# Optimization experiments

Hardware: AMD Instinct MI355X
Metric: run time of the kernel (lower is better)

## Reference

```python
import jax, jax.numpy as jnp
import numpy as np

N = 10000        # total_node
IN_SIZE = 128
OUT_SIZE = 128


def setup_inputs() -> dict:
    key = jax.random.key(0)
    k_adj, k_x, k_wn, k_ws = jax.random.split(key, 4)
    adj = jax.random.uniform(k_adj, (N, N), dtype=jnp.float32)           # package[1]
    old_node_embedding = jax.random.normal(k_x, (N, IN_SIZE), dtype=jnp.float32)
    # nn.Linear weights are stored [out, in]
    W_nei = jax.random.normal(k_wn, (OUT_SIZE, IN_SIZE), dtype=jnp.float32) * (1.0 / np.sqrt(IN_SIZE))
    W_self = jax.random.normal(k_ws, (OUT_SIZE, IN_SIZE), dtype=jnp.float32) * (1.0 / np.sqrt(IN_SIZE))
    return {
        "adj": adj,
        "old_node_embedding": old_node_embedding,
        "W_nei": W_nei,
        "W_self": W_self,
        "out_size": OUT_SIZE,
        "use_divce": 0,
    }


def reference(adj, old_node_embedding, W_nei, W_self, out_size, use_divce):
    # Vectorized form of the per-node torch loop:
    #   nei_gather[n]   = adj[n, :] @ X                (torch.mm per node)
    #   nei_info[n]     = nei_gather[n] @ W_nei^T      (nei_update1)
    #   self_info[n]    = X[n] @ W_self^T              (self_node_update1)
    #   new_emb[n]      = act(nei_info[n] + self_info[n])
    # active_method fixed to tanh.
    nei_gather = adj @ old_node_embedding                         # [N, in]
    nei_info = nei_gather @ W_nei.T                               # [N, out]
    self_info = old_node_embedding @ W_self.T                     # [N, out]
    return jnp.tanh(nei_info + self_info)
```

## Files before the change

kernel.cpp:

```cpp
#include <hip/hip_runtime.h>
#include <cmath>


#define N_NODES 10000
#define EMB 128
#define XNT_STRIDE 10240
#define KC 1280
#define NKCH 8

typedef __bf16 bf16x8 __attribute__((ext_vector_type(8)));
typedef float  f32x4  __attribute__((ext_vector_type(4)));

#define GLOAD_LDS16(gp, lp)                                                  \
    __builtin_amdgcn_global_load_lds(                                        \
        (const __attribute__((address_space(1))) void*)(gp),                 \
        (__attribute__((address_space(3))) void*)(lp), 16, 0, 0)

__device__ __forceinline__ void split8(const float4& x0, const float4& x1,
                                       bf16x8& h, bf16x8& l) {
    float f[8] = {x0.x, x0.y, x0.z, x0.w, x1.x, x1.y, x1.z, x1.w};
#pragma unroll
    for (int i = 0; i < 8; ++i) {
        __bf16 hh = (__bf16)f[i];
        h[i] = hh;
        l[i] = (__bf16)(f[i] - (float)hh);
    }
}

__global__ __launch_bounds__(256) void prep_kernel(
    const float* __restrict__ X, const float* __restrict__ Wn,
    __bf16* __restrict__ xnt_hi, __bf16* __restrict__ xnt_lo)
{
    __shared__ float Xl[32 * EMB];
    const int tid = threadIdx.x;
    const int n0 = blockIdx.x * 32;

    if (blockIdx.x == 0) {
        bf16x8 z;
#pragma unroll
        for (int i = 0; i < 8; ++i) z[i] = (__bf16)0.0f;
        for (int g = tid; g < 128 * 30; g += 256) {
            int col = g / 30, j = g % 30;
            size_t off = (size_t)col * XNT_STRIDE + N_NODES + j * 8;
            *(bf16x8*)(xnt_hi + off) = z;
            *(bf16x8*)(xnt_lo + off) = z;
        }
    }

#pragma unroll
    for (int i = 0; i < 4; ++i) {
        int idx = tid + i * 256;
        int r = idx >> 5;
        int c4 = (idx & 31) << 2;
        int row = n0 + r;
        float4 v = make_float4(0.f, 0.f, 0.f, 0.f);
        if (row < N_NODES) v = *(const float4*)(X + (size_t)row * EMB + c4);
        *(float4*)(Xl + r * EMB + c4) = v;
    }
    __syncthreads();

    const int c = tid & 127;
    const int half = tid >> 7;
    const float* wrow = Wn + c * EMB;

    float acc[16];
#pragma unroll
    for (int r = 0; r < 16; ++r) acc[r] = 0.f;

    for (int k4 = 0; k4 < 32; ++k4) {
        float4 w = *(const float4*)(wrow + k4 * 4);
#pragma unroll
        for (int r = 0; r < 16; ++r) {
            float4 x = *(const float4*)(Xl + (half * 16 + r) * EMB + k4 * 4);
            acc[r] += x.x * w.x + x.y * w.y + x.z * w.z + x.w * w.w;
        }
    }

    if (n0 + half * 16 < N_NODES) {
        bf16x8 h0, h1, l0, l1;
#pragma unroll
        for (int r = 0; r < 16; ++r) {
            float f = acc[r];
            __bf16 h = (__bf16)f;
            __bf16 l = (__bf16)(f - (float)h);
            if (r < 8) { h0[r] = h; l0[r] = l; }
            else       { h1[r - 8] = h; l1[r - 8] = l; }
        }
        size_t base = (size_t)c * XNT_STRIDE + n0 + half * 16;
        *(bf16x8*)(xnt_hi + base)     = h0;
        *(bf16x8*)(xnt_hi + base + 8) = h1;
        *(bf16x8*)(xnt_lo + base)     = l0;
        *(bf16x8*)(xnt_lo + base + 8) = l1;
    }
}

__global__ __launch_bounds__(256, 4) void gemm_kernel(
    const float* __restrict__ adj, const __bf16* __restrict__ xnt_hi,
    const __bf16* __restrict__ xnt_lo, float* __restrict__ Ppart)
{
    __shared__ float  Af [64 * 32];
    __shared__ __bf16 Bhs[128 * 32];
    __shared__ __bf16 Bls[128 * 32];

    const int tid = threadIdx.x;
    const int m0 = blockIdx.x * 64;
    const int kc0 = blockIdx.y * KC;
    const int kc_end = min(kc0 + KC, N_NODES);
    const int nsub = (kc_end - kc0 + 31) >> 5;

    const int lane = tid & 63;
    const int wave = tid >> 6;
    const int wm = (wave & 1) * 32;
    const int wn = (wave >> 1) * 64;
    const int fr = lane & 15;
    const int q  = lane >> 4;
    const int f7 = fr & 7;

    const int a_c4 = ((tid & 7) ^ ((tid >> 3) & 7)) * 4;
    size_t a_rowoff[2];
#pragma unroll
    for (int i = 0; i < 2; ++i) {
        int r = i * 32 + (tid >> 3);
        if (m0 + r >= N_NODES) r &= 15;
        a_rowoff[i] = (size_t)(m0 + r) * N_NODES;
    }
    const int b_k8 = ((tid & 3) ^ ((tid >> 3) & 3)) * 8;
    size_t b_coloff[2];
#pragma unroll
    for (int i = 0; i < 2; ++i)
        b_coloff[i] = (size_t)(i * 64 + (tid >> 2)) * XNT_STRIDE;

    f32x4 acc[2][4];
#pragma unroll
    for (int mt = 0; mt < 2; ++mt)
#pragma unroll
        for (int nt = 0; nt < 4; ++nt)
#pragma unroll
            for (int e = 0; e < 4; ++e) acc[mt][nt][e] = 0.f;

    for (int ks = 0; ks < nsub; ++ks) {
        const int k0 = kc0 + ks * 32;

#pragma unroll
        for (int i = 0; i < 2; ++i) {
            int kk = k0 + a_c4;
            if (kk + 4 > kc_end) kk = kc0;
            GLOAD_LDS16(adj + a_rowoff[i] + kk, Af + (i * 256 + tid) * 4);
        }
#pragma unroll
        for (int i = 0; i < 2; ++i) {
            GLOAD_LDS16(xnt_hi + b_coloff[i] + k0 + b_k8,
                        Bhs + (i * 256 + tid) * 8);
            GLOAD_LDS16(xnt_lo + b_coloff[i] + k0 + b_k8,
                        Bls + (i * 256 + tid) * 8);
        }
        __syncthreads();

        bf16x8 ah[2], al[2], bh[4], bl[4];
#pragma unroll
        for (int mt = 0; mt < 2; ++mt) {
            int r = wm + mt * 16 + fr;
            int c0 = q * 2;
            int pc0 = c0 ^ f7;
            int pc1 = (c0 + 1) ^ f7;
            float4 fa = *(const float4*)(Af + r * 32 + pc0 * 4);
            float4 fb = *(const float4*)(Af + r * 32 + pc1 * 4);
            split8(fa, fb, ah[mt], al[mt]);
        }
#pragma unroll
        for (int nt = 0; nt < 4; ++nt) {
            int col = wn + nt * 16 + fr;
            int pq = q ^ ((fr >> 1) & 3);
            bh[nt] = *(const bf16x8*)(Bhs + col * 32 + pq * 8);
            bl[nt] = *(const bf16x8*)(Bls + col * 32 + pq * 8);
        }
#pragma unroll
        for (int mt = 0; mt < 2; ++mt)
#pragma unroll
            for (int nt = 0; nt < 4; ++nt) {
                acc[mt][nt] = __builtin_amdgcn_mfma_f32_16x16x32_bf16(ah[mt], bh[nt], acc[mt][nt], 0, 0, 0);
                acc[mt][nt] = __builtin_amdgcn_mfma_f32_16x16x32_bf16(ah[mt], bl[nt], acc[mt][nt], 0, 0, 0);
                acc[mt][nt] = __builtin_amdgcn_mfma_f32_16x16x32_bf16(al[mt], bh[nt], acc[mt][nt], 0, 0, 0);
            }

        __syncthreads();
    }

    float* P = Ppart + (size_t)blockIdx.y * ((size_t)N_NODES * EMB);
#pragma unroll
    for (int mt = 0; mt < 2; ++mt) {
        int rbase = m0 + wm + mt * 16 + q * 4;
#pragma unroll
        for (int nt = 0; nt < 4; ++nt) {
            int col = wn + nt * 16 + fr;
#pragma unroll
            for (int r = 0; r < 4; ++r) {
                int row = rbase + r;
                if (row < N_NODES)
                    P[(size_t)row * EMB + col] = acc[mt][nt][r];
            }
        }
    }
}

__global__ __launch_bounds__(256) void epi_kernel(
    const float* __restrict__ X, const float* __restrict__ Wself,
    const float* __restrict__ Ppart, float* __restrict__ out)
{
    __shared__ float Xl[32 * EMB];
    const int tid = threadIdx.x;
    const int n0 = blockIdx.x * 32;

#pragma unroll
    for (int i = 0; i < 4; ++i) {
        int idx = tid + i * 256;
        int r = idx >> 5;
        int c4 = (idx & 31) << 2;
        int row = n0 + r;
        float4 v = make_float4(0.f, 0.f, 0.f, 0.f);
        if (row < N_NODES) v = *(const float4*)(X + (size_t)row * EMB + c4);
        *(float4*)(Xl + r * EMB + c4) = v;
    }
    __syncthreads();

    const int c = tid & 127;
    const int half = tid >> 7;
    const float* wrow = Wself + c * EMB;

    float acc[16];
#pragma unroll
    for (int r = 0; r < 16; ++r) acc[r] = 0.f;

    for (int k4 = 0; k4 < 32; ++k4) {
        float4 w = *(const float4*)(wrow + k4 * 4);
#pragma unroll
        for (int r = 0; r < 16; ++r) {
            float4 x = *(const float4*)(Xl + (half * 16 + r) * EMB + k4 * 4);
            acc[r] += x.x * w.x + x.y * w.y + x.z * w.z + x.w * w.w;
        }
    }

    if (n0 + half * 16 < N_NODES) {
        const size_t rb = (size_t)(n0 + half * 16) * EMB + c;
#pragma unroll
        for (int p = 0; p < NKCH; ++p) {
            const float* Pp = Ppart + (size_t)p * ((size_t)N_NODES * EMB) + rb;
#pragma unroll
            for (int r = 0; r < 16; ++r)
                acc[r] += Pp[(size_t)r * EMB];
        }
#pragma unroll
        for (int r = 0; r < 16; ++r)
            out[rb + (size_t)r * EMB] = tanhf(acc[r]);
    }
}

__global__ __launch_bounds__(256) void gemm0_kernel(
    const float* __restrict__ adj, const float* __restrict__ X,
    float* __restrict__ Y)
{
    __shared__ float As[128 * 33];
    __shared__ float Xs[32 * 132];
    const int tid = threadIdx.x;
    const int m0 = blockIdx.x * 128;
    const int kc0 = blockIdx.y * KC;
    const int kc_end = min(kc0 + KC, N_NODES);
    const int nsub = (kc_end - kc0 + 31) >> 5;

    const int am = tid >> 1, akq = tid & 1;
    const bool arv = (m0 + am) < N_NODES;
    const float* arow_p = adj + (size_t)(m0 + am) * N_NODES;
    const int xr = tid >> 3, xq = tid & 7;
    const int mq = tid >> 4, nq = tid & 15;

    float acc[8][8];
#pragma unroll
    for (int i = 0; i < 8; ++i)
#pragma unroll
        for (int j = 0; j < 8; ++j) acc[i][j] = 0.f;

    for (int ks = 0; ks < nsub; ++ks) {
        int k0 = kc0 + ks * 32;
#pragma unroll
        for (int i = 0; i < 4; ++i) {
            int k = k0 + akq * 16 + i * 4;
            float4 v = make_float4(0.f, 0.f, 0.f, 0.f);
            if (arv && k < kc_end) v = *(const float4*)(arow_p + k);
            float* d = As + am * 33 + akq * 16 + i * 4;
            d[0] = v.x; d[1] = v.y; d[2] = v.z; d[3] = v.w;
        }
#pragma unroll
        for (int i = 0; i < 4; ++i) {
            int c0 = xq * 16 + i * 4;
            int krow = k0 + xr;
            float4 v = make_float4(0.f, 0.f, 0.f, 0.f);
            if (krow < kc_end) v = *(const float4*)(X + (size_t)krow * EMB + c0);
            *(float4*)(Xs + xr * 132 + c0) = v;
        }
        __syncthreads();
        for (int k = 0; k < 32; ++k) {
            float a8[8];
#pragma unroll
            for (int i = 0; i < 8; ++i) a8[i] = As[(mq * 8 + i) * 33 + k];
            float4 x0 = *(const float4*)(Xs + k * 132 + nq * 8);
            float4 x1 = *(const float4*)(Xs + k * 132 + nq * 8 + 4);
            float x8[8] = { x0.x, x0.y, x0.z, x0.w, x1.x, x1.y, x1.z, x1.w };
#pragma unroll
            for (int i = 0; i < 8; ++i)
#pragma unroll
                for (int j = 0; j < 8; ++j) acc[i][j] += a8[i] * x8[j];
        }
        __syncthreads();
    }
#pragma unroll
    for (int i = 0; i < 8; ++i) {
        int row = m0 + mq * 8 + i;
        if (row < N_NODES) {
#pragma unroll
            for (int j = 0; j < 8; ++j)
                atomicAdd(Y + (size_t)row * EMB + nq * 8 + j, acc[i][j]);
        }
    }
}

__global__ __launch_bounds__(256) void epi0_kernel(
    const float* __restrict__ X, const float* __restrict__ Wn,
    const float* __restrict__ Ws, float* __restrict__ out)
{
    __shared__ float Xl[32 * EMB];
    __shared__ float Yl[32 * EMB];
    const int tid = threadIdx.x;
    const int n0 = blockIdx.x * 32;

#pragma unroll
    for (int i = 0; i < 4; ++i) {
        int idx = tid + i * 256;
        int r = idx >> 5;
        int c4 = (idx & 31) << 2;
        int row = n0 + r;
        float4 vx = make_float4(0.f, 0.f, 0.f, 0.f);
        float4 vy = vx;
        if (row < N_NODES) {
            vx = *(const float4*)(X + (size_t)row * EMB + c4);
            vy = *(const float4*)(out + (size_t)row * EMB + c4);
        }
        *(float4*)(Xl + r * EMB + c4) = vx;
        *(float4*)(Yl + r * EMB + c4) = vy;
    }
    __syncthreads();

    const int c = tid & 127;
    const int half = tid >> 7;
    const float* wn = Wn + c * EMB;
    const float* ws = Ws + c * EMB;

    float accn[16], accs[16];
#pragma unroll
    for (int r = 0; r < 16; ++r) { accn[r] = 0.f; accs[r] = 0.f; }

    for (int k4 = 0; k4 < 32; ++k4) {
        float4 a = *(const float4*)(wn + k4 * 4);
        float4 b = *(const float4*)(ws + k4 * 4);
#pragma unroll
        for (int r = 0; r < 16; ++r) {
            float4 y = *(const float4*)(Yl + (half * 16 + r) * EMB + k4 * 4);
            float4 x = *(const float4*)(Xl + (half * 16 + r) * EMB + k4 * 4);
            accn[r] += y.x * a.x + y.y * a.y + y.z * a.z + y.w * a.w;
            accs[r] += x.x * b.x + x.y * b.y + x.z * b.z + x.w * b.w;
        }
    }
#pragma unroll
    for (int r = 0; r < 16; ++r) {
        int row = n0 + half * 16 + r;
        if (row < N_NODES)
            out[(size_t)row * EMB + c] = tanhf(accn[r] + accs[r]);
    }
}

extern "C" void kernel_launch(void* const* d_in, const int* in_sizes, int n_in,
                              void* d_out, int out_size, void* d_ws, size_t ws_size,
                              hipStream_t stream) {
    const float* adj = (const float*)d_in[0];
    const float* X   = (const float*)d_in[1];
    const float* Wn  = (const float*)d_in[2];
    const float* Ws  = (const float*)d_in[3];
    float* out = (float*)d_out;

    const size_t xnt_elems = (size_t)EMB * XNT_STRIDE;
    const size_t xnt_bytes = xnt_elems * 2 * sizeof(unsigned short);
    const size_t part_bytes = (size_t)NKCH * N_NODES * EMB * sizeof(float);

    if (ws_size >= xnt_bytes + part_bytes) {
        __bf16* xh = (__bf16*)d_ws;
        __bf16* xl = xh + xnt_elems;
        float* Ppart = (float*)((char*)d_ws + xnt_bytes);
        prep_kernel<<<(N_NODES + 31) / 32, 256, 0, stream>>>(X, Wn, xh, xl);
        gemm_kernel<<<dim3((N_NODES + 63) / 64, NKCH), 256, 0, stream>>>(adj, xh, xl, Ppart);
        epi_kernel<<<(N_NODES + 31) / 32, 256, 0, stream>>>(X, Ws, Ppart, out);
    } else {
        hipMemsetAsync(d_out, 0, (size_t)N_NODES * EMB * sizeof(float), stream);
        gemm0_kernel<<<dim3((N_NODES + 127) / 128, NKCH), 256, 0, stream>>>(adj, X, out);
        epi0_kernel<<<(N_NODES + 31) / 32, 256, 0, stream>>>(X, Wn, Ws, out);
    }
}
```

Measured before the change: 642.3 us.

## Drop LDS staging in adjacency GEMM, load fragments directly from global memory

The GEMM kernel no longer stages adj and the bf16 hi/lo X tiles in shared memory with global_load_lds and barriers. Each wave now reads its MFMA fragments straight from global memory, and the block tile grows to 128 rows by the full 128 columns, with each wave owning 32 rows across all columns. This removes the LDS round trip and the __syncthreads calls. In exchange, each wave does uncoalesced strided global loads of the B fragments, every wave rereads the same B data and relies on cache, registers per thread rise, and the occupancy hint is dropped.

```diff
diff --git a/kernel.cpp b/kernel.cpp
--- a/kernel.cpp
+++ b/kernel.cpp
@@ -10,11 +10,6 @@
 
 typedef __bf16 bf16x8 __attribute__((ext_vector_type(8)));
 typedef float  f32x4  __attribute__((ext_vector_type(4)));
-
-#define GLOAD_LDS16(gp, lp)                                                  \
-    __builtin_amdgcn_global_load_lds(                                        \
-        (const __attribute__((address_space(1))) void*)(gp),                 \
-        (__attribute__((address_space(3))) void*)(lp), 16, 0, 0)
 
 __device__ __forceinline__ void split8(const float4& x0, const float4& x1,
                                        bf16x8& h, bf16x8& l) {
@@ -94,96 +89,75 @@
     }
 }
 
-__global__ __launch_bounds__(256, 4) void gemm_kernel(
+__global__ __launch_bounds__(256) void gemm_kernel(
     const float* __restrict__ adj, const __bf16* __restrict__ xnt_hi,
     const __bf16* __restrict__ xnt_lo, float* __restrict__ Ppart)
 {
-    __shared__ float  Af [64 * 32];
-    __shared__ __bf16 Bhs[128 * 32];
-    __shared__ __bf16 Bls[128 * 32];
-
-    const int tid = threadIdx.x;
-    const int m0 = blockIdx.x * 64;
+    const int tid = threadIdx.x;
+    const int m0 = blockIdx.x * 128;
     const int kc0 = blockIdx.y * KC;
     const int kc_end = min(kc0 + KC, N_NODES);
     const int nsub = (kc_end - kc0 + 31) >> 5;
 
     const int lane = tid & 63;
     const int wave = tid >> 6;
-    const int wm = (wave & 1) * 32;
-    const int wn = (wave >> 1) * 64;
+    const int wm = wave * 32;
     const int fr = lane & 15;
     const int q  = lane >> 4;
-    const int f7 = fr & 7;
-
-    const int a_c4 = ((tid & 7) ^ ((tid >> 3) & 7)) * 4;
-    size_t a_rowoff[2];
-#pragma unroll
-    for (int i = 0; i < 2; ++i) {
-        int r = i * 32 + (tid >> 3);
-        if (m0 + r >= N_NODES) r &= 15;
-        a_rowoff[i] = (size_t)(m0 + r) * N_NODES;
-    }
-    const int b_k8 = ((tid & 3) ^ ((tid >> 3) & 3)) * 8;
-    size_t b_coloff[2];
-#pragma unroll
-    for (int i = 0; i < 2; ++i)
-        b_coloff[i] = (size_t)(i * 64 + (tid >> 2)) * XNT_STRIDE;
-
-    f32x4 acc[2][4];
+
+    const float* arow[2];
+#pragma unroll
+    for (int mt = 0; mt < 2; ++mt) {
+        int r = m0 + wm + mt * 16 + fr;
+        if (r >= N_NODES) r = 0;
+        arow[mt] = adj + (size_t)r * N_NODES;
+    }
+
+    size_t bcol[8];
+#pragma unroll
+    for (int nt = 0; nt < 8; ++nt)
+        bcol[nt] = (size_t)(nt * 16 + fr) * XNT_STRIDE;
+
+    f32x4 acc[2][8];
 #pragma unroll
     for (int mt = 0; mt < 2; ++mt)
 #pragma unroll
-        for (int nt = 0; nt < 4; ++nt)
+        for (int nt = 0; nt < 8; ++nt)
 #pragma unroll
             for (int e = 0; e < 4; ++e) acc[mt][nt][e] = 0.f;
 
     for (int ks = 0; ks < nsub; ++ks) {
         const int k0 = kc0 + ks * 32;
-
-#pragma unroll
-        for (int i = 0; i < 2; ++i) {
-            int kk = k0 + a_c4;
-            if (kk + 4 > kc_end) kk = kc0;
-            GLOAD_LDS16(adj + a_rowoff[i] + kk, Af + (i * 256 + tid) * 4);
-        }
-#pragma unroll
-        for (int i = 0; i < 2; ++i) {
-            GLOAD_LDS16(xnt_hi + b_coloff[i] + k0 + b_k8,
-                        Bhs + (i * 256 + tid) * 8);
-            GLOAD_LDS16(xnt_lo + b_coloff[i] + k0 + b_k8,
-                        Bls + (i * 256 + tid) * 8);
-        }
-        __syncthreads();
-
-        bf16x8 ah[2], al[2], bh[4], bl[4];
+        const int ka = k0 + q * 8;
+        const int kaA = (ka >= kc_end) ? kc0 : ka;
+
+        bf16x8 ah[2], al[2];
 #pragma unroll
         for (int mt = 0; mt < 2; ++mt) {
-            int r = wm + mt * 16 + fr;
-            int c0 = q * 2;
-            int pc0 = c0 ^ f7;
-            int pc1 = (c0 + 1) ^ f7;
-            float4 fa = *(const float4*)(Af + r * 32 + pc0 * 4);
-            float4 fb = *(const float4*)(Af + r * 32 + pc1 * 4);
+            float4 fa = *(const float4*)(arow[mt] + kaA);
+            float4 fb = *(const float4*)(arow[mt] + kaA + 4);
             split8(fa, fb, ah[mt], al[mt]);
         }
-#pragma unroll
-        for (int nt = 0; nt < 4; ++nt) {
-            int col = wn + nt * 16 + fr;
-            int pq = q ^ ((fr >> 1) & 3);
-            bh[nt] = *(const bf16x8*)(Bhs + col * 32 + pq * 8);
-            bl[nt] = *(const bf16x8*)(Bls + col * 32 + pq * 8);
-        }
-#pragma unroll
-        for (int mt = 0; mt < 2; ++mt)
-#pragma unroll
-            for (int nt = 0; nt < 4; ++nt) {
-                acc[mt][nt] = __builtin_amdgcn_mfma_f32_16x16x32_bf16(ah[mt], bh[nt], acc[mt][nt], 0, 0, 0);
-                acc[mt][nt] = __builtin_amdgcn_mfma_f32_16x16x32_bf16(ah[mt], bl[nt], acc[mt][nt], 0, 0, 0);
-                acc[mt][nt] = __builtin_amdgcn_mfma_f32_16x16x32_bf16(al[mt], bh[nt], acc[mt][nt], 0, 0, 0);
+
+#pragma unroll
+        for (int h = 0; h < 2; ++h) {
+            bf16x8 bh[4], bl[4];
+#pragma unroll
+            for (int j = 0; j < 4; ++j) {
+                size_t boff = bcol[h * 4 + j] + ka;
+                bh[j] = *(const bf16x8*)(xnt_hi + boff);
+                bl[j] = *(const bf16x8*)(xnt_lo + boff);
             }
-
-        __syncthreads();
+#pragma unroll
+            for (int mt = 0; mt < 2; ++mt)
+#pragma unroll
+                for (int j = 0; j < 4; ++j) {
+                    const int nt = h * 4 + j;
+                    acc[mt][nt] = __builtin_amdgcn_mfma_f32_16x16x32_bf16(ah[mt], bh[j], acc[mt][nt], 0, 0, 0);
+                    acc[mt][nt] = __builtin_amdgcn_mfma_f32_16x16x32_bf16(ah[mt], bl[j], acc[mt][nt], 0, 0, 0);
+                    acc[mt][nt] = __builtin_amdgcn_mfma_f32_16x16x32_bf16(al[mt], bh[j], acc[mt][nt], 0, 0, 0);
+                }
+        }
     }
 
     float* P = Ppart + (size_t)blockIdx.y * ((size_t)N_NODES * EMB);
@@ -191,8 +165,8 @@
     for (int mt = 0; mt < 2; ++mt) {
         int rbase = m0 + wm + mt * 16 + q * 4;
 #pragma unroll
-        for (int nt = 0; nt < 4; ++nt) {
-            int col = wn + nt * 16 + fr;
+        for (int nt = 0; nt < 8; ++nt) {
+            int col = nt * 16 + fr;
 #pragma unroll
             for (int r = 0; r < 4; ++r) {
                 int row = rbase + r;
@@ -395,7 +369,7 @@
         __bf16* xl = xh + xnt_elems;
         float* Ppart = (float*)((char*)d_ws + xnt_bytes);
         prep_kernel<<<(N_NODES + 31) / 32, 256, 0, stream>>>(X, Wn, xh, xl);
-        gemm_kernel<<<dim3((N_NODES + 63) / 64, NKCH), 256, 0, stream>>>(adj, xh, xl, Ppart);
+        gemm_kernel<<<dim3((N_NODES + 127) / 128, NKCH), 256, 0, stream>>>(adj, xh, xl, Ppart);
         epi_kernel<<<(N_NODES + 31) / 32, 256, 0, stream>>>(X, Ws, Ppart, out);
     } else {
         hipMemsetAsync(d_out, 0, (size_t)N_NODES * EMB * sizeof(float), stream);
```

After: 799.6 us. 24.5% more time.
